# Optimization experiments

Measured on AMD Instinct MI355X. Metric: run time of the kernel, lower is better.

Reference implementation:

```python
import jax, jax.numpy as jnp
import numpy as np

B = 1      # batch
D = 64     # octree grid side at this level
N = 65536  # active voxels
C = 32     # channels (nin == nout for resblock)
K = 3      # kernel size


def _offsets():
    r = jnp.arange(K) - K // 2
    oz, oy, ox = jnp.meshgrid(r, r, r, indexing='ij')
    return jnp.stack([oz.ravel(), oy.ravel(), ox.ravel()], axis=-1)  # [27,3] (kz,ky,kx order)


def octree_conv3d(values, indices, mask_values, kernel, bias, activation=None):
    # values: [N,Cin], indices: [N,4] (b,z,y,x), mask_values: [N,1]
    Cin = values.shape[-1]
    Cout = kernel.shape[-1]
    taps = kernel.reshape(K * K * K, Cin, Cout)            # kz,ky,kx order == kernel[kz,ky,kx]
    vals = jnp.einsum('nc,tcd->tnd', values, taps)         # [27,N,Cout]
    offs = _offsets()                                      # [27,3]
    coords = indices[:, 1:]                                # [N,3]
    # shift = [0, kz-1, ky-1, kx-1]; clamp to [0, D-1] (stride=inv_stride=1)
    sh = jnp.clip(coords[None, :, :] + offs[:, None, :], 0, D - 1)  # [27,N,3]
    lin = indices[:, 0][None, :] * (D * D * D) + sh[..., 0] * (D * D) + sh[..., 1] * D + sh[..., 2]
    grid = jnp.zeros((B * D * D * D, Cout), dtype=values.dtype)
    grid = grid.at[lin.reshape(-1)].add(vals.reshape(-1, Cout))     # scatter-add == coalesce sum
    out_lin = indices[:, 0] * (D * D * D) + coords[:, 0] * (D * D) + coords[:, 1] * D + coords[:, 2]
    gathered = grid[out_lin]                               # [N,Cout] values at mask positions
    out = (gathered + mask_values * bias[None, :]) * mask_values     # result + mask*bias; result*mask
    if activation is not None:
        out = activation(out)
    return out


def setup_inputs() -> dict:
    key = jax.random.key(0)
    k1, k2, k3, k4, k5, k6 = jax.random.split(key, 6)
    G = B * D * D * D
    perm = jax.random.permutation(k1, G)[:N]               # unique (coalesced) voxel indices
    b = perm // (D * D * D)
    rem = perm % (D * D * D)
    z = rem // (D * D)
    y = (rem // D) % D
    x = rem % D
    indices = jnp.stack([b, z, y, x], axis=-1).astype(jnp.int64)   # [N,4]
    values = jax.random.normal(k2, (N, C), dtype=jnp.float32)
    mask_values = jnp.ones((N, 1), dtype=jnp.float32)
    stdv = 1.0 / np.sqrt(K * K * K * C)
    kern1 = (jax.random.uniform(k3, (K, K, K, C, C)) - 0.5) * 2.0 * stdv
    bias1 = (jax.random.uniform(k4, (C,)) - 0.5) * 2.0 * stdv
    kern2 = (jax.random.uniform(k5, (K, K, K, C, C)) - 0.5) * 2.0 * stdv
    bias2 = (jax.random.uniform(k6, (C,)) - 0.5) * 2.0 * stdv
    return {'values': values, 'indices': indices, 'mask_values': mask_values,
            'kern1': kern1, 'bias1': bias1, 'kern2': kern2, 'bias2': bias2}


def reference(values, indices, mask_values, kern1, bias1, kern2, bias2):
    # OctreeResblock: conv(relu) -> conv -> residual add, all on the sparse index set
    h = octree_conv3d(values, indices, mask_values, kern1, bias1, activation=jax.nn.relu)
    h = octree_conv3d(h, indices, mask_values, kern2, bias2, activation=None)
    return values + h
```

## Files before the change

kernel.cpp:

```cpp
#include <hip/hip_runtime.h>

#define NPTS 65536
#define CCH  32
#define DDIM 64
#define GVOX (DDIM*DDIM*DDIM)
#define MAXTILES 4128

typedef _Float16 half8  __attribute__((ext_vector_type(8)));
typedef _Float16 half4v __attribute__((ext_vector_type(4)));
typedef float    floatx4 __attribute__((ext_vector_type(4)));

__global__ __launch_bounds__(256) void k_prep0(
    int* __restrict__ map, int* __restrict__ sorted,
    const float* __restrict__ values, _Float16* __restrict__ valsh,
    const float* __restrict__ k1, const float* __restrict__ k2,
    _Float16* __restrict__ w1, _Float16* __restrict__ w2,
    _Float16* __restrict__ hh, int* __restrict__ pcoord,
    int* __restrict__ cnt, int* __restrict__ slot)
{
  int tid = blockIdx.x * 256 + threadIdx.x;
  if (tid < GVOX/4) { ((int4*)map)[tid] = make_int4(-1,-1,-1,-1); return; }
  tid -= GVOX/4;
  if (tid < MAXTILES*16) { sorted[tid] = NPTS; return; }
  tid -= MAXTILES*16;
  if (tid < (NPTS*CCH)/4) {
    float4 v = ((const float4*)values)[tid];
    half4v h = { (_Float16)v.x, (_Float16)v.y, (_Float16)v.z, (_Float16)v.w };
    ((half4v*)valsh)[tid] = h; return;
  }
  tid -= (NPTS*CCH)/4;
  if (tid < 27*CCH*CCH) {
    int t = tid/(CCH*CCH), r = tid%(CCH*CCH);
    int cin = r/CCH, cout = r%CCH;
    int o = (t*CCH + cout)*CCH + cin;
    w1[o] = (_Float16)k1[tid]; w2[o] = (_Float16)k2[tid]; return;
  }
  tid -= 27*CCH*CCH;
  if (tid < CCH) { valsh[NPTS*CCH+tid] = (_Float16)0.f; hh[NPTS*CCH+tid] = (_Float16)0.f; return; }
  tid -= CCH;
  if (tid < 27) { cnt[tid] = 0; slot[tid] = 0; return; }
  tid -= 27;
  if (tid == 0) pcoord[NPTS] = 0;
}
#define PREP0_THREADS (GVOX/4 + MAXTILES*16 + (NPTS*CCH)/4 + 27*CCH*CCH + CCH + 27 + 1)

__global__ __launch_bounds__(256) void k_prep1(const int* __restrict__ idx,
                                               int* __restrict__ map,
                                               int* __restrict__ pcoord,
                                               int* __restrict__ cls,
                                               int* __restrict__ cnt)
{
  __shared__ int lcnt[27];
  if (threadIdx.x < 27) lcnt[threadIdx.x] = 0;
  __syncthreads();
  const int n = blockIdx.x*256 + threadIdx.x;
  const int4 v = ((const int4*)idx)[n];
  const int b = v.x, z = v.y, y = v.z, x = v.w;
  map[((b*DDIM + z)*DDIM + y)*DDIM + x] = n;
  pcoord[n] = (b<<18) | (z<<12) | (y<<6) | x;
  const int cz = (z==0)?0:((z==DDIM-1)?2:1);
  const int cy = (y==0)?0:((y==DDIM-1)?2:1);
  const int cx = (x==0)?0:((x==DDIM-1)?2:1);
  const int c = cz*9 + cy*3 + cx;
  cls[n] = c;
  atomicAdd(&lcnt[c], 1);
  __syncthreads();
  if (threadIdx.x < 27 && lcnt[threadIdx.x]) atomicAdd(&cnt[threadIdx.x], lcnt[threadIdx.x]);
}

__global__ __launch_bounds__(256) void k_prep3(const int* __restrict__ cls,
                                               const int* __restrict__ cnt,
                                               int* __restrict__ slot,
                                               int* __restrict__ sorted,
                                               int* __restrict__ tileclass,
                                               int* __restrict__ ntiles)
{
  __shared__ int s_clsbase[27];
  __shared__ int s_tstart[28];
  if (threadIdx.x == 0) {
    int b = 0, tb = 0;
#pragma unroll
    for (int c = 0; c < 27; ++c) {
      s_clsbase[c] = b; s_tstart[c] = tb;
      const int ntc = (cnt[c] + 15) >> 4;
      b += ntc << 4; tb += ntc;
    }
    s_tstart[27] = tb;
    if (blockIdx.x == 0) *ntiles = tb;
  }
  __syncthreads();

  if (blockIdx.x < NPTS/256) {
    __shared__ int lcnt[27], lbase[27];
    if (threadIdx.x < 27) lcnt[threadIdx.x] = 0;
    __syncthreads();
    const int n = blockIdx.x*256 + threadIdx.x;
    const int c = cls[n];
    const int lrank = atomicAdd(&lcnt[c], 1);
    __syncthreads();
    if (threadIdx.x < 27)
      lbase[threadIdx.x] = lcnt[threadIdx.x] ? atomicAdd(&slot[threadIdx.x], lcnt[threadIdx.x]) : 0;
    __syncthreads();
    sorted[s_clsbase[c] + lbase[c] + lrank] = n;
  } else {
    const int i = (blockIdx.x - NPTS/256)*256 + threadIdx.x;
    if (i >= MAXTILES) return;
    const int nt = s_tstart[27];
    int c = 13;
    if (i < nt) {
      for (int cc = 0; cc < 27; ++cc)
        if (i >= s_tstart[cc] && i < s_tstart[cc+1]) { c = cc; break; }
    }
    tileclass[i] = c;
  }
}

template<int J0, int J1>
__device__ __forceinline__ void accum_taps(
    const _Float16* __restrict__ A, const int* __restrict__ map,
    const _Float16* __restrict__ WT,
    int cz, int cy, int cx, int linb,
    const int* az, const int* ay, const int* ax,
    int m, int quad, floatx4& acc0, floatx4& acc1)
{
  int srcs[J1 - J0];
#pragma unroll
  for (int j = J0; j < J1; ++j) {
    const int jz = j/9, jy = (j/3)%3, jx = j%3;
    const int s = map[linb | az[jz] | ay[jy] | ax[jx]];
    srcs[j - J0] = (s < 0) ? (NPTS*CCH) : (s*CCH);
  }
#pragma unroll
  for (int j = J0; j < J1; ++j) {
    const int jz = j/9, jy = (j/3)%3, jx = j%3;
    const int tz = (cz==1) ? (2-jz) : ((jz==1) ? 1 : ((cz==0) ? 0 : 2));
    const int ty = (cy==1) ? (2-jy) : ((jy==1) ? 1 : ((cy==0) ? 0 : 2));
    const int tx = (cx==1) ? (2-jx) : ((jx==1) ? 1 : ((cx==0) ? 0 : 2));
    const int t  = tz*9 + ty*3 + tx;
    half8 a  = *(const half8*)(A + srcs[j - J0] + quad*8);
    const _Float16* wr = WT + t*(CCH*CCH);
    half8 b0 = *(const half8*)(wr + m*CCH + quad*8);
    half8 b1 = *(const half8*)(wr + (16+m)*CCH + quad*8);
    acc0 = __builtin_amdgcn_mfma_f32_16x16x32_f16(a, b0, acc0, 0, 0, 0);
    acc1 = __builtin_amdgcn_mfma_f32_16x16x32_f16(a, b1, acc1, 0, 0, 0);
  }
}

template<int MODE>
__global__ __launch_bounds__(256) void conv_mfma(
    const _Float16* __restrict__ A,
    const int* __restrict__ map,
    const int* __restrict__ pcoord,
    const int* __restrict__ sorted,
    const int* __restrict__ tileclass,
    const int* __restrict__ ntp,
    const _Float16* __restrict__ WT,
    const float* __restrict__ bias,
    const float* __restrict__ mask,
    const float* __restrict__ resid,
    _Float16* __restrict__ hout,
    float* __restrict__ fout)
{
  __shared__ float red[2][16][33];
  const int wv   = threadIdx.x >> 6;
  const int tl   = wv >> 1;
  const int half = wv & 1;
  const int tile = blockIdx.x*2 + tl;
  const int nt   = *ntp;
  const bool active = tile < nt;
  const int lane = threadIdx.x & 63;
  const int m = lane & 15, quad = lane >> 4;

  floatx4 acc0 = {0.f,0.f,0.f,0.f};
  floatx4 acc1 = {0.f,0.f,0.f,0.f};

  if (active) {
    const int scls = __builtin_amdgcn_readfirstlane(tileclass[tile]);
    const int cz = scls/9, cy = (scls/3)%3, cx = scls%3;
    const int pid = sorted[tile*16 + m];
    const int pc  = pcoord[pid];
    const int bb = pc>>18, z = (pc>>12)&63, y = (pc>>6)&63, x = pc&63;
    const int linb = bb << 18;
    const int az[3] = { max(z-1,0)<<12, z<<12, min(z+1,DDIM-1)<<12 };
    const int ay[3] = { max(y-1,0)<<6,  y<<6,  min(y+1,DDIM-1)<<6 };
    const int ax[3] = { max(x-1,0),     x,     min(x+1,DDIM-1) };
    if (half == 0)
      accum_taps<0,14>(A, map, WT, cz,cy,cx, linb, az,ay,ax, m,quad, acc0,acc1);
    else
      accum_taps<14,27>(A, map, WT, cz,cy,cx, linb, az,ay,ax, m,quad, acc0,acc1);
  }

  if (active && half == 0) {
#pragma unroll
    for (int r = 0; r < 4; ++r) {
      red[tl][quad*4+r][m]    = acc0[r];
      red[tl][quad*4+r][m+16] = acc1[r];
    }
  }
  __syncthreads();
  if (active && half == 1) {
#pragma unroll
    for (int r = 0; r < 4; ++r) {
      acc0[r] += red[tl][quad*4+r][m];
      acc1[r] += red[tl][quad*4+r][m+16];
    }
    const float bi0 = bias[m], bi1 = bias[m+16];
#pragma unroll
    for (int reg = 0; reg < 4; ++reg) {
      const int r  = quad*4 + reg;
      const int pr = sorted[tile*16 + r];
      if (pr >= NPTS) continue;
      const float mk = mask[pr];
      float v0 = (acc0[reg] + mk*bi0) * mk;
      float v1 = (acc1[reg] + mk*bi1) * mk;
      if (MODE == 0) {
        v0 = fmaxf(v0, 0.f); v1 = fmaxf(v1, 0.f);
        hout[pr*CCH + m]      = (_Float16)v0;
        hout[pr*CCH + m + 16] = (_Float16)v1;
      } else {
        fout[pr*CCH + m]      = resid[pr*CCH + m]      + v0;
        fout[pr*CCH + m + 16] = resid[pr*CCH + m + 16] + v1;
      }
    }
  }
}


extern "C" void kernel_launch(void* const* d_in, const int* in_sizes, int n_in,
                              void* d_out, int out_size, void* d_ws, size_t ws_size,
                              hipStream_t stream) {
  const float* values = (const float*)d_in[0];
  const int*   indices= (const int*)  d_in[1];
  const float* maskv  = (const float*)d_in[2];
  const float* kern1  = (const float*)d_in[3];
  const float* bias1  = (const float*)d_in[4];
  const float* kern2  = (const float*)d_in[5];
  const float* bias2  = (const float*)d_in[6];
  float* out = (float*)d_out;

  char* ws = (char*)d_ws;
  size_t off = 0;
  auto alloc = [&](size_t bytes) { void* p = ws + off; off = (off + bytes + 255) & ~(size_t)255; return p; };
  int*      map      = (int*)     alloc(GVOX*4);
  int*      pcoord   = (int*)     alloc((NPTS+1)*4);
  int*      cls      = (int*)     alloc(NPTS*4);
  int*      sorted   = (int*)     alloc(MAXTILES*16*4);
  int*      tileclass= (int*)     alloc(MAXTILES*4);
  int*      cnt      = (int*)     alloc(27*4);
  int*      slot     = (int*)     alloc(27*4);
  int*      ntiles   = (int*)     alloc(4);
  _Float16* valsh    = (_Float16*)alloc((NPTS+1)*CCH*2);
  _Float16* hh       = (_Float16*)alloc((NPTS+1)*CCH*2);
  _Float16* wt1      = (_Float16*)alloc(27*CCH*CCH*2);
  _Float16* wt2      = (_Float16*)alloc(27*CCH*CCH*2);

  k_prep0<<<(PREP0_THREADS + 255)/256, 256, 0, stream>>>(
      map, sorted, values, valsh, kern1, kern2, wt1, wt2, hh, pcoord, cnt, slot);
  k_prep1<<<NPTS/256, 256, 0, stream>>>(indices, map, pcoord, cls, cnt);
  k_prep3<<<NPTS/256 + (MAXTILES+255)/256, 256, 0, stream>>>(
      cls, cnt, slot, sorted, tileclass, ntiles);

  conv_mfma<0><<<MAXTILES/2, 256, 0, stream>>>(valsh, map, pcoord, sorted, tileclass,
                                               ntiles, wt1, bias1, maskv, nullptr, hh, nullptr);
  conv_mfma<1><<<MAXTILES/2, 256, 0, stream>>>(hh, map, pcoord, sorted, tileclass,
                                               ntiles, wt2, bias2, maskv, values, nullptr, out);
}
```

Before: 145.1 us.

## Sort voxels by boundary class and spatial cell, store features in slot order

Points are keyed by boundary class plus an 8x8x8 spatial cell and counting-sorted through a new single-block scan kernel. The voxel map, fp16 features, and intermediate activations are then stored in sorted-slot order, so neighbour gathers in the conv kernels touch nearby memory and the pcoord indirection goes away. This adds a launch and a serial single-block scan over 13.8K keys. Atomic ordering within a cell is nondeterministic.

```diff
diff --git a/kernel.cpp b/kernel.cpp
--- a/kernel.cpp
+++ b/kernel.cpp
@@ -5,30 +5,28 @@
 #define DDIM 64
 #define GVOX (DDIM*DDIM*DDIM)
 #define MAXTILES 4128
+#define NSLOTCAP (MAXTILES*16)
+#define NCELL 512
+#define KEYS (27*NCELL)
+#define CHUNK (KEYS/256)
 
 typedef _Float16 half8  __attribute__((ext_vector_type(8)));
-typedef _Float16 half4v __attribute__((ext_vector_type(4)));
 typedef float    floatx4 __attribute__((ext_vector_type(4)));
 
 __global__ __launch_bounds__(256) void k_prep0(
-    int* __restrict__ map, int* __restrict__ sorted,
-    const float* __restrict__ values, _Float16* __restrict__ valsh,
+    int* __restrict__ map, int* __restrict__ sorted, int* __restrict__ pcoords,
     const float* __restrict__ k1, const float* __restrict__ k2,
     _Float16* __restrict__ w1, _Float16* __restrict__ w2,
-    _Float16* __restrict__ hh, int* __restrict__ pcoord,
-    int* __restrict__ cnt, int* __restrict__ slot)
+    _Float16* __restrict__ valsh, _Float16* __restrict__ hh,
+    int* __restrict__ cntslot)
 {
   int tid = blockIdx.x * 256 + threadIdx.x;
   if (tid < GVOX/4) { ((int4*)map)[tid] = make_int4(-1,-1,-1,-1); return; }
   tid -= GVOX/4;
-  if (tid < MAXTILES*16) { sorted[tid] = NPTS; return; }
-  tid -= MAXTILES*16;
-  if (tid < (NPTS*CCH)/4) {
-    float4 v = ((const float4*)values)[tid];
-    half4v h = { (_Float16)v.x, (_Float16)v.y, (_Float16)v.z, (_Float16)v.w };
-    ((half4v*)valsh)[tid] = h; return;
-  }
-  tid -= (NPTS*CCH)/4;
+  if (tid < MAXTILES*4) { ((int4*)sorted)[tid] = make_int4(NPTS,NPTS,NPTS,NPTS); return; }
+  tid -= MAXTILES*4;
+  if (tid < MAXTILES*4) { ((int4*)pcoords)[tid] = make_int4(0,0,0,0); return; }
+  tid -= MAXTILES*4;
   if (tid < 27*CCH*CCH) {
     int t = tid/(CCH*CCH), r = tid%(CCH*CCH);
     int cin = r/CCH, cout = r%CCH;
@@ -36,80 +34,114 @@
     w1[o] = (_Float16)k1[tid]; w2[o] = (_Float16)k2[tid]; return;
   }
   tid -= 27*CCH*CCH;
-  if (tid < CCH) { valsh[NPTS*CCH+tid] = (_Float16)0.f; hh[NPTS*CCH+tid] = (_Float16)0.f; return; }
+  if (tid < CCH) {
+    valsh[NSLOTCAP*CCH + tid] = (_Float16)0.f;
+    hh[NSLOTCAP*CCH + tid]    = (_Float16)0.f; return;
+  }
   tid -= CCH;
-  if (tid < 27) { cnt[tid] = 0; slot[tid] = 0; return; }
-  tid -= 27;
-  if (tid == 0) pcoord[NPTS] = 0;
-}
-#define PREP0_THREADS (GVOX/4 + MAXTILES*16 + (NPTS*CCH)/4 + 27*CCH*CCH + CCH + 27 + 1)
+  if (tid < (2*KEYS)/4) { ((int4*)cntslot)[tid] = make_int4(0,0,0,0); return; }
+}
+#define PREP0_THREADS (GVOX/4 + MAXTILES*4 + MAXTILES*4 + 27*CCH*CCH + CCH + (2*KEYS)/4)
 
 __global__ __launch_bounds__(256) void k_prep1(const int* __restrict__ idx,
-                                               int* __restrict__ map,
-                                               int* __restrict__ pcoord,
-                                               int* __restrict__ cls,
+                                               int* __restrict__ key,
+                                               int* __restrict__ pk,
                                                int* __restrict__ cnt)
 {
-  __shared__ int lcnt[27];
-  if (threadIdx.x < 27) lcnt[threadIdx.x] = 0;
-  __syncthreads();
   const int n = blockIdx.x*256 + threadIdx.x;
   const int4 v = ((const int4*)idx)[n];
   const int b = v.x, z = v.y, y = v.z, x = v.w;
-  map[((b*DDIM + z)*DDIM + y)*DDIM + x] = n;
-  pcoord[n] = (b<<18) | (z<<12) | (y<<6) | x;
+  pk[n] = (b<<18) | (z<<12) | (y<<6) | x;
   const int cz = (z==0)?0:((z==DDIM-1)?2:1);
   const int cy = (y==0)?0:((y==DDIM-1)?2:1);
   const int cx = (x==0)?0:((x==DDIM-1)?2:1);
   const int c = cz*9 + cy*3 + cx;
-  cls[n] = c;
-  atomicAdd(&lcnt[c], 1);
-  __syncthreads();
-  if (threadIdx.x < 27 && lcnt[threadIdx.x]) atomicAdd(&cnt[threadIdx.x], lcnt[threadIdx.x]);
-}
-
-__global__ __launch_bounds__(256) void k_prep3(const int* __restrict__ cls,
-                                               const int* __restrict__ cnt,
+  const int cell = ((z>>3)<<6) | ((y>>3)<<3) | (x>>3);
+  const int k = (c<<9) | cell;
+  key[n] = k;
+  atomicAdd(&cnt[k], 1);
+}
+
+__global__ __launch_bounds__(256) void k_scan(const int* __restrict__ cnt,
+                                              int* __restrict__ keybase,
+                                              int* __restrict__ tstart,
+                                              int* __restrict__ ntiles)
+{
+  __shared__ int E[KEYS];
+  __shared__ int ts[256];
+  __shared__ int clsb[27], clsu[27];
+  const int t = threadIdx.x;
+  int run = 0;
+  for (int i = 0; i < CHUNK; ++i) {
+    const int k = t*CHUNK + i;
+    const int v = cnt[k];
+    E[k] = run; run += v;
+  }
+  ts[t] = run;
+  __syncthreads();
+  if (t == 0) {
+    int r = 0;
+    for (int i = 0; i < 256; ++i) { const int v = ts[i]; ts[i] = r; r += v; }
+  }
+  __syncthreads();
+  const int off = ts[t];
+  for (int i = 0; i < CHUNK; ++i) E[t*CHUNK + i] += off;
+  __syncthreads();
+  if (t == 0) {
+    int b = 0, tb = 0;
+    for (int c = 0; c < 27; ++c) {
+      const int start = E[c*NCELL];
+      const int end   = (c == 26) ? NPTS : E[(c+1)*NCELL];
+      clsu[c] = start; clsb[c] = b; tstart[c] = tb;
+      const int ntc = (end - start + 15) >> 4;
+      b += ntc << 4; tb += ntc;
+    }
+    tstart[27] = tb; *ntiles = tb;
+  }
+  __syncthreads();
+  for (int i = 0; i < CHUNK; ++i) {
+    const int k = t*CHUNK + i, c = k >> 9;
+    keybase[k] = clsb[c] + (E[k] - clsu[c]);
+  }
+}
+
+__global__ __launch_bounds__(256) void k_prep3(const int* __restrict__ key,
+                                               const int* __restrict__ pk,
+                                               const float* __restrict__ values,
+                                               const int* __restrict__ keybase,
                                                int* __restrict__ slot,
                                                int* __restrict__ sorted,
+                                               int* __restrict__ map,
+                                               int* __restrict__ pcoords,
+                                               _Float16* __restrict__ valsh,
+                                               const int* __restrict__ tstart,
                                                int* __restrict__ tileclass,
-                                               int* __restrict__ ntiles)
-{
-  __shared__ int s_clsbase[27];
-  __shared__ int s_tstart[28];
-  if (threadIdx.x == 0) {
-    int b = 0, tb = 0;
-#pragma unroll
-    for (int c = 0; c < 27; ++c) {
-      s_clsbase[c] = b; s_tstart[c] = tb;
-      const int ntc = (cnt[c] + 15) >> 4;
-      b += ntc << 4; tb += ntc;
-    }
-    s_tstart[27] = tb;
-    if (blockIdx.x == 0) *ntiles = tb;
-  }
-  __syncthreads();
-
+                                               const int* __restrict__ ntp)
+{
   if (blockIdx.x < NPTS/256) {
-    __shared__ int lcnt[27], lbase[27];
-    if (threadIdx.x < 27) lcnt[threadIdx.x] = 0;
-    __syncthreads();
     const int n = blockIdx.x*256 + threadIdx.x;
-    const int c = cls[n];
-    const int lrank = atomicAdd(&lcnt[c], 1);
-    __syncthreads();
-    if (threadIdx.x < 27)
-      lbase[threadIdx.x] = lcnt[threadIdx.x] ? atomicAdd(&slot[threadIdx.x], lcnt[threadIdx.x]) : 0;
-    __syncthreads();
-    sorted[s_clsbase[c] + lbase[c] + lrank] = n;
+    const int k = key[n], p = pk[n];
+    const int s = keybase[k] + atomicAdd(&slot[k], 1);
+    sorted[s] = n;
+    pcoords[s] = p;
+    map[p] = s;
+    const float4* src = (const float4*)(values + n*CCH);
+    half8* dst = (half8*)(valsh + s*CCH);
+#pragma unroll
+    for (int i = 0; i < 4; ++i) {
+      float4 a = src[2*i], b = src[2*i+1];
+      half8 h = {(_Float16)a.x,(_Float16)a.y,(_Float16)a.z,(_Float16)a.w,
+                 (_Float16)b.x,(_Float16)b.y,(_Float16)b.z,(_Float16)b.w};
+      dst[i] = h;
+    }
   } else {
     const int i = (blockIdx.x - NPTS/256)*256 + threadIdx.x;
     if (i >= MAXTILES) return;
-    const int nt = s_tstart[27];
+    const int nt = *ntp;
     int c = 13;
     if (i < nt) {
       for (int cc = 0; cc < 27; ++cc)
-        if (i >= s_tstart[cc] && i < s_tstart[cc+1]) { c = cc; break; }
+        if (i >= tstart[cc] && i < tstart[cc+1]) { c = cc; break; }
     }
     tileclass[i] = c;
   }
@@ -128,7 +160,7 @@
   for (int j = J0; j < J1; ++j) {
     const int jz = j/9, jy = (j/3)%3, jx = j%3;
     const int s = map[linb | az[jz] | ay[jy] | ax[jx]];
-    srcs[j - J0] = (s < 0) ? (NPTS*CCH) : (s*CCH);
+    srcs[j - J0] = (s < 0) ? (NSLOTCAP*CCH) : (s*CCH);
   }
 #pragma unroll
   for (int j = J0; j < J1; ++j) {
@@ -150,7 +182,7 @@
 __global__ __launch_bounds__(256) void conv_mfma(
     const _Float16* __restrict__ A,
     const int* __restrict__ map,
-    const int* __restrict__ pcoord,
+    const int* __restrict__ pcoords,
     const int* __restrict__ sorted,
     const int* __restrict__ tileclass,
     const int* __restrict__ ntp,
@@ -177,8 +209,7 @@
   if (active) {
     const int scls = __builtin_amdgcn_readfirstlane(tileclass[tile]);
     const int cz = scls/9, cy = (scls/3)%3, cx = scls%3;
-    const int pid = sorted[tile*16 + m];
-    const int pc  = pcoord[pid];
+    const int pc = pcoords[tile*16 + m];
     const int bb = pc>>18, z = (pc>>12)&63, y = (pc>>6)&63, x = pc&63;
     const int linb = bb << 18;
     const int az[3] = { max(z-1,0)<<12, z<<12, min(z+1,DDIM-1)<<12 };
@@ -207,16 +238,17 @@
     const float bi0 = bias[m], bi1 = bias[m+16];
 #pragma unroll
     for (int reg = 0; reg < 4; ++reg) {
-      const int r  = quad*4 + reg;
-      const int pr = sorted[tile*16 + r];
+      const int r    = quad*4 + reg;
+      const int srow = tile*16 + r;
+      const int pr   = sorted[srow];
       if (pr >= NPTS) continue;
       const float mk = mask[pr];
       float v0 = (acc0[reg] + mk*bi0) * mk;
       float v1 = (acc1[reg] + mk*bi1) * mk;
       if (MODE == 0) {
         v0 = fmaxf(v0, 0.f); v1 = fmaxf(v1, 0.f);
-        hout[pr*CCH + m]      = (_Float16)v0;
-        hout[pr*CCH + m + 16] = (_Float16)v1;
+        hout[srow*CCH + m]      = (_Float16)v0;
+        hout[srow*CCH + m + 16] = (_Float16)v1;
       } else {
         fout[pr*CCH + m]      = resid[pr*CCH + m]      + v0;
         fout[pr*CCH + m + 16] = resid[pr*CCH + m + 16] + v1;
@@ -242,26 +274,32 @@
   size_t off = 0;
   auto alloc = [&](size_t bytes) { void* p = ws + off; off = (off + bytes + 255) & ~(size_t)255; return p; };
   int*      map      = (int*)     alloc(GVOX*4);
-  int*      pcoord   = (int*)     alloc((NPTS+1)*4);
-  int*      cls      = (int*)     alloc(NPTS*4);
-  int*      sorted   = (int*)     alloc(MAXTILES*16*4);
+  int*      key      = (int*)     alloc(NPTS*4);
+  int*      pk       = (int*)     alloc(NPTS*4);
+  int*      sorted   = (int*)     alloc(NSLOTCAP*4);
+  int*      pcoords  = (int*)     alloc(NSLOTCAP*4);
   int*      tileclass= (int*)     alloc(MAXTILES*4);
-  int*      cnt      = (int*)     alloc(27*4);
-  int*      slot     = (int*)     alloc(27*4);
+  int*      cntslot  = (int*)     alloc(2*KEYS*4);
+  int*      keybase  = (int*)     alloc(KEYS*4);
+  int*      tstart   = (int*)     alloc(28*4);
   int*      ntiles   = (int*)     alloc(4);
-  _Float16* valsh    = (_Float16*)alloc((NPTS+1)*CCH*2);
-  _Float16* hh       = (_Float16*)alloc((NPTS+1)*CCH*2);
+  _Float16* valsh    = (_Float16*)alloc((size_t)(NSLOTCAP+1)*CCH*2);
+  _Float16* hh       = (_Float16*)alloc((size_t)(NSLOTCAP+1)*CCH*2);
   _Float16* wt1      = (_Float16*)alloc(27*CCH*CCH*2);
   _Float16* wt2      = (_Float16*)alloc(27*CCH*CCH*2);
+  int* cnt  = cntslot;
+  int* slot = cntslot + KEYS;
 
   k_prep0<<<(PREP0_THREADS + 255)/256, 256, 0, stream>>>(
-      map, sorted, values, valsh, kern1, kern2, wt1, wt2, hh, pcoord, cnt, slot);
-  k_prep1<<<NPTS/256, 256, 0, stream>>>(indices, map, pcoord, cls, cnt);
+      map, sorted, pcoords, kern1, kern2, wt1, wt2, valsh, hh, cntslot);
+  k_prep1<<<NPTS/256, 256, 0, stream>>>(indices, key, pk, cnt);
+  k_scan<<<1, 256, 0, stream>>>(cnt, keybase, tstart, ntiles);
   k_prep3<<<NPTS/256 + (MAXTILES+255)/256, 256, 0, stream>>>(
-      cls, cnt, slot, sorted, tileclass, ntiles);
-
-  conv_mfma<0><<<MAXTILES/2, 256, 0, stream>>>(valsh, map, pcoord, sorted, tileclass,
+      key, pk, values, keybase, slot, sorted, map, pcoords, valsh,
+      tstart, tileclass, ntiles);
+
+  conv_mfma<0><<<MAXTILES/2, 256, 0, stream>>>(valsh, map, pcoords, sorted, tileclass,
                                                ntiles, wt1, bias1, maskv, nullptr, hh, nullptr);
-  conv_mfma<1><<<MAXTILES/2, 256, 0, stream>>>(hh, map, pcoord, sorted, tileclass,
+  conv_mfma<1><<<MAXTILES/2, 256, 0, stream>>>(hh, map, pcoords, sorted, tileclass,
                                                ntiles, wt2, bias2, maskv, values, nullptr, out);
 }
```

Result: slower. 184.2 us (+26.9%).

## Precompute neighbor table once, stage weights in LDS, one wave per tile

Applied to the files above, without the earlier changes.

Adds a k_nbr kernel that builds a per-tile neighbor offset table once, reused by both convolutions. This replaces the per-conv hash-map lookups on voxel coordinates. The conv kernel now copies all 27 taps of fp16 weights (about 55KB) into shared memory in an MFMA-friendly swizzled layout, and processes one tile per wave with 8 waves per block, which removes the two-wave split-tap reduction through LDS. The trade-offs are an extra kernel launch, a roughly 7MB neighbor table round trip through memory, and a large LDS footprint that may limit occupancy.

```diff
diff --git a/kernel.cpp b/kernel.cpp
--- a/kernel.cpp
+++ b/kernel.cpp
@@ -5,13 +5,14 @@
 #define DDIM 64
 #define GVOX (DDIM*DDIM*DDIM)
 #define MAXTILES 4128
+#define NSLOT (MAXTILES*16)
 
 typedef _Float16 half8  __attribute__((ext_vector_type(8)));
 typedef _Float16 half4v __attribute__((ext_vector_type(4)));
 typedef float    floatx4 __attribute__((ext_vector_type(4)));
 
 __global__ __launch_bounds__(256) void k_prep0(
-    int* __restrict__ map, int* __restrict__ sorted,
+    int* __restrict__ map, int* __restrict__ sorted, int* __restrict__ pcs,
     const float* __restrict__ values, _Float16* __restrict__ valsh,
     const float* __restrict__ k1, const float* __restrict__ k2,
     _Float16* __restrict__ w1, _Float16* __restrict__ w2,
@@ -21,8 +22,10 @@
   int tid = blockIdx.x * 256 + threadIdx.x;
   if (tid < GVOX/4) { ((int4*)map)[tid] = make_int4(-1,-1,-1,-1); return; }
   tid -= GVOX/4;
-  if (tid < MAXTILES*16) { sorted[tid] = NPTS; return; }
-  tid -= MAXTILES*16;
+  if (tid < NSLOT) { sorted[tid] = NPTS; return; }
+  tid -= NSLOT;
+  if (tid < NSLOT) { pcs[tid] = 0; return; }
+  tid -= NSLOT;
   if (tid < (NPTS*CCH)/4) {
     float4 v = ((const float4*)values)[tid];
     half4v h = { (_Float16)v.x, (_Float16)v.y, (_Float16)v.z, (_Float16)v.w };
@@ -32,7 +35,8 @@
   if (tid < 27*CCH*CCH) {
     int t = tid/(CCH*CCH), r = tid%(CCH*CCH);
     int cin = r/CCH, cout = r%CCH;
-    int o = (t*CCH + cout)*CCH + cin;
+    int h = cout >> 4, mm = cout & 15, q = cin >> 3, i = cin & 7;
+    int o = t*1024 + h*512 + (q*16 + mm)*8 + i;
     w1[o] = (_Float16)k1[tid]; w2[o] = (_Float16)k2[tid]; return;
   }
   tid -= 27*CCH*CCH;
@@ -42,7 +46,7 @@
   tid -= 27;
   if (tid == 0) pcoord[NPTS] = 0;
 }
-#define PREP0_THREADS (GVOX/4 + MAXTILES*16 + (NPTS*CCH)/4 + 27*CCH*CCH + CCH + 27 + 1)
+#define PREP0_THREADS (GVOX/4 + NSLOT + NSLOT + (NPTS*CCH)/4 + 27*CCH*CCH + CCH + 27 + 1)
 
 __global__ __launch_bounds__(256) void k_prep1(const int* __restrict__ idx,
                                                int* __restrict__ map,
@@ -71,7 +75,9 @@
 __global__ __launch_bounds__(256) void k_prep3(const int* __restrict__ cls,
                                                const int* __restrict__ cnt,
                                                int* __restrict__ slot,
+                                               const int* __restrict__ pcoord,
                                                int* __restrict__ sorted,
+                                               int* __restrict__ pcs,
                                                int* __restrict__ tileclass,
                                                int* __restrict__ ntiles)
 {
@@ -101,7 +107,9 @@
     if (threadIdx.x < 27)
       lbase[threadIdx.x] = lcnt[threadIdx.x] ? atomicAdd(&slot[threadIdx.x], lcnt[threadIdx.x]) : 0;
     __syncthreads();
-    sorted[s_clsbase[c] + lbase[c] + lrank] = n;
+    const int s = s_clsbase[c] + lbase[c] + lrank;
+    sorted[s] = n;
+    pcs[s] = pcoord[n];
   } else {
     const int i = (blockIdx.x - NPTS/256)*256 + threadIdx.x;
     if (i >= MAXTILES) return;
@@ -115,42 +123,28 @@
   }
 }
 
-template<int J0, int J1>
-__device__ __forceinline__ void accum_taps(
-    const _Float16* __restrict__ A, const int* __restrict__ map,
-    const _Float16* __restrict__ WT,
-    int cz, int cy, int cx, int linb,
-    const int* az, const int* ay, const int* ax,
-    int m, int quad, floatx4& acc0, floatx4& acc1)
-{
-  int srcs[J1 - J0];
-#pragma unroll
-  for (int j = J0; j < J1; ++j) {
-    const int jz = j/9, jy = (j/3)%3, jx = j%3;
-    const int s = map[linb | az[jz] | ay[jy] | ax[jx]];
-    srcs[j - J0] = (s < 0) ? (NPTS*CCH) : (s*CCH);
-  }
-#pragma unroll
-  for (int j = J0; j < J1; ++j) {
-    const int jz = j/9, jy = (j/3)%3, jx = j%3;
-    const int tz = (cz==1) ? (2-jz) : ((jz==1) ? 1 : ((cz==0) ? 0 : 2));
-    const int ty = (cy==1) ? (2-jy) : ((jy==1) ? 1 : ((cy==0) ? 0 : 2));
-    const int tx = (cx==1) ? (2-jx) : ((jx==1) ? 1 : ((cx==0) ? 0 : 2));
-    const int t  = tz*9 + ty*3 + tx;
-    half8 a  = *(const half8*)(A + srcs[j - J0] + quad*8);
-    const _Float16* wr = WT + t*(CCH*CCH);
-    half8 b0 = *(const half8*)(wr + m*CCH + quad*8);
-    half8 b1 = *(const half8*)(wr + (16+m)*CCH + quad*8);
-    acc0 = __builtin_amdgcn_mfma_f32_16x16x32_f16(a, b0, acc0, 0, 0, 0);
-    acc1 = __builtin_amdgcn_mfma_f32_16x16x32_f16(a, b1, acc1, 0, 0, 0);
-  }
+__global__ __launch_bounds__(256) void k_nbr(const int* __restrict__ pcs,
+                                             const int* __restrict__ map,
+                                             int* __restrict__ nbr)
+{
+  const int tid = blockIdx.x*256 + threadIdx.x;
+  if (tid >= MAXTILES*432) return;
+  const int tile = tid/432, rem = tid%432;
+  const int j = rem >> 4, m = rem & 15;
+  const int pc = pcs[tile*16 + m];
+  const int bb = pc>>18, z = (pc>>12)&63, y = (pc>>6)&63, x = pc&63;
+  const int jz = j/9, jy = (j/3)%3, jx = j%3;
+  const int nz = min(max(z + jz - 1, 0), DDIM-1);
+  const int ny = min(max(y + jy - 1, 0), DDIM-1);
+  const int nx = min(max(x + jx - 1, 0), DDIM-1);
+  const int s = map[(bb<<18) | (nz<<12) | (ny<<6) | nx];
+  nbr[tid] = ((s < 0) ? NPTS : s) * CCH;
 }
 
 template<int MODE>
-__global__ __launch_bounds__(256) void conv_mfma(
+__global__ __launch_bounds__(512, 4) void conv_mfma(
     const _Float16* __restrict__ A,
-    const int* __restrict__ map,
-    const int* __restrict__ pcoord,
+    const int* __restrict__ nbr,
     const int* __restrict__ sorted,
     const int* __restrict__ tileclass,
     const int* __restrict__ ntp,
@@ -161,66 +155,66 @@
     _Float16* __restrict__ hout,
     float* __restrict__ fout)
 {
-  __shared__ float red[2][16][33];
+  __shared__ _Float16 lw[27*CCH*CCH];
+  for (int i = threadIdx.x; i < 3456; i += 512)
+    ((half8*)lw)[i] = ((const half8*)WT)[i];
+  __syncthreads();
+
   const int wv   = threadIdx.x >> 6;
-  const int tl   = wv >> 1;
-  const int half = wv & 1;
-  const int tile = blockIdx.x*2 + tl;
-  const int nt   = *ntp;
-  const bool active = tile < nt;
+  const int tile = blockIdx.x*8 + wv;
   const int lane = threadIdx.x & 63;
   const int m = lane & 15, quad = lane >> 4;
+  if (tile >= *ntp) return;
+
+  const int scls = __builtin_amdgcn_readfirstlane(tileclass[tile]);
+  const int cz = scls/9, cy = (scls/3)%3, cx = scls%3;
+
+  const int tb = tile*432;
+  int srcs[27];
+#pragma unroll
+  for (int j = 0; j < 27; ++j) srcs[j] = nbr[tb + j*16 + m];
 
   floatx4 acc0 = {0.f,0.f,0.f,0.f};
   floatx4 acc1 = {0.f,0.f,0.f,0.f};
 
-  if (active) {
-    const int scls = __builtin_amdgcn_readfirstlane(tileclass[tile]);
-    const int cz = scls/9, cy = (scls/3)%3, cx = scls%3;
-    const int pid = sorted[tile*16 + m];
-    const int pc  = pcoord[pid];
-    const int bb = pc>>18, z = (pc>>12)&63, y = (pc>>6)&63, x = pc&63;
-    const int linb = bb << 18;
-    const int az[3] = { max(z-1,0)<<12, z<<12, min(z+1,DDIM-1)<<12 };
-    const int ay[3] = { max(y-1,0)<<6,  y<<6,  min(y+1,DDIM-1)<<6 };
-    const int ax[3] = { max(x-1,0),     x,     min(x+1,DDIM-1) };
-    if (half == 0)
-      accum_taps<0,14>(A, map, WT, cz,cy,cx, linb, az,ay,ax, m,quad, acc0,acc1);
-    else
-      accum_taps<14,27>(A, map, WT, cz,cy,cx, linb, az,ay,ax, m,quad, acc0,acc1);
-  }
-
-  if (active && half == 0) {
-#pragma unroll
-    for (int r = 0; r < 4; ++r) {
-      red[tl][quad*4+r][m]    = acc0[r];
-      red[tl][quad*4+r][m+16] = acc1[r];
-    }
-  }
-  __syncthreads();
-  if (active && half == 1) {
-#pragma unroll
-    for (int r = 0; r < 4; ++r) {
-      acc0[r] += red[tl][quad*4+r][m];
-      acc1[r] += red[tl][quad*4+r][m+16];
-    }
-    const float bi0 = bias[m], bi1 = bias[m+16];
-#pragma unroll
-    for (int reg = 0; reg < 4; ++reg) {
-      const int r  = quad*4 + reg;
-      const int pr = sorted[tile*16 + r];
-      if (pr >= NPTS) continue;
-      const float mk = mask[pr];
-      float v0 = (acc0[reg] + mk*bi0) * mk;
-      float v1 = (acc1[reg] + mk*bi1) * mk;
-      if (MODE == 0) {
-        v0 = fmaxf(v0, 0.f); v1 = fmaxf(v1, 0.f);
-        hout[pr*CCH + m]      = (_Float16)v0;
-        hout[pr*CCH + m + 16] = (_Float16)v1;
-      } else {
-        fout[pr*CCH + m]      = resid[pr*CCH + m]      + v0;
-        fout[pr*CCH + m + 16] = resid[pr*CCH + m + 16] + v1;
-      }
+#pragma unroll
+  for (int g = 0; g < 3; ++g) {
+    half8 av[9];
+#pragma unroll
+    for (int u = 0; u < 9; ++u)
+      av[u] = *(const half8*)(A + srcs[g*9 + u] + quad*8);
+#pragma unroll
+    for (int u = 0; u < 9; ++u) {
+      const int j = g*9 + u;
+      const int jz = j/9, jy = (j/3)%3, jx = j%3;
+      const int tz = (cz==1) ? (2-jz) : ((jz==1) ? 1 : ((cz==0) ? 0 : 2));
+      const int ty = (cy==1) ? (2-jy) : ((jy==1) ? 1 : ((cy==0) ? 0 : 2));
+      const int tx = (cx==1) ? (2-jx) : ((jx==1) ? 1 : ((cx==0) ? 0 : 2));
+      const int t  = tz*9 + ty*3 + tx;
+      const _Float16* wr = lw + t*1024;
+      half8 b0 = *(const half8*)(wr + lane*8);
+      half8 b1 = *(const half8*)(wr + 512 + lane*8);
+      acc0 = __builtin_amdgcn_mfma_f32_16x16x32_f16(av[u], b0, acc0, 0, 0, 0);
+      acc1 = __builtin_amdgcn_mfma_f32_16x16x32_f16(av[u], b1, acc1, 0, 0, 0);
+    }
+  }
+
+  const float bi0 = bias[m], bi1 = bias[m+16];
+#pragma unroll
+  for (int reg = 0; reg < 4; ++reg) {
+    const int r  = quad*4 + reg;
+    const int pr = sorted[tile*16 + r];
+    if (pr >= NPTS) continue;
+    const float mk = mask[pr];
+    float v0 = (acc0[reg] + mk*bi0) * mk;
+    float v1 = (acc1[reg] + mk*bi1) * mk;
+    if (MODE == 0) {
+      v0 = fmaxf(v0, 0.f); v1 = fmaxf(v1, 0.f);
+      hout[pr*CCH + m]      = (_Float16)v0;
+      hout[pr*CCH + m + 16] = (_Float16)v1;
+    } else {
+      fout[pr*CCH + m]      = resid[pr*CCH + m]      + v0;
+      fout[pr*CCH + m + 16] = resid[pr*CCH + m + 16] + v1;
     }
   }
 }
@@ -244,8 +238,10 @@
   int*      map      = (int*)     alloc(GVOX*4);
   int*      pcoord   = (int*)     alloc((NPTS+1)*4);
   int*      cls      = (int*)     alloc(NPTS*4);
-  int*      sorted   = (int*)     alloc(MAXTILES*16*4);
+  int*      sorted   = (int*)     alloc(NSLOT*4);
+  int*      pcs      = (int*)     alloc(NSLOT*4);
   int*      tileclass= (int*)     alloc(MAXTILES*4);
+  int*      nbr      = (int*)     alloc((size_t)MAXTILES*432*4);
   int*      cnt      = (int*)     alloc(27*4);
   int*      slot     = (int*)     alloc(27*4);
   int*      ntiles   = (int*)     alloc(4);
@@ -255,13 +251,14 @@
   _Float16* wt2      = (_Float16*)alloc(27*CCH*CCH*2);
 
   k_prep0<<<(PREP0_THREADS + 255)/256, 256, 0, stream>>>(
-      map, sorted, values, valsh, kern1, kern2, wt1, wt2, hh, pcoord, cnt, slot);
+      map, sorted, pcs, values, valsh, kern1, kern2, wt1, wt2, hh, pcoord, cnt, slot);
   k_prep1<<<NPTS/256, 256, 0, stream>>>(indices, map, pcoord, cls, cnt);
   k_prep3<<<NPTS/256 + (MAXTILES+255)/256, 256, 0, stream>>>(
-      cls, cnt, slot, sorted, tileclass, ntiles);
-
-  conv_mfma<0><<<MAXTILES/2, 256, 0, stream>>>(valsh, map, pcoord, sorted, tileclass,
-                                               ntiles, wt1, bias1, maskv, nullptr, hh, nullptr);
-  conv_mfma<1><<<MAXTILES/2, 256, 0, stream>>>(hh, map, pcoord, sorted, tileclass,
-                                               ntiles, wt2, bias2, maskv, values, nullptr, out);
-}
+      cls, cnt, slot, pcoord, sorted, pcs, tileclass, ntiles);
+  k_nbr<<<(MAXTILES*432 + 255)/256, 256, 0, stream>>>(pcs, map, nbr);
+
+  conv_mfma<0><<<(MAXTILES + 7)/8, 512, 0, stream>>>(valsh, nbr, sorted, tileclass,
+                                                     ntiles, wt1, bias1, maskv, nullptr, hh, nullptr);
+  conv_mfma<1><<<(MAXTILES + 7)/8, 512, 0, stream>>>(hh, nbr, sorted, tileclass,
+                                                     ntiles, wt2, bias2, maskv, values, nullptr, out);
+}
```

Result: faster. 128.6 us (-11.3%).
